# Performance work log

Hardware: AMD Instinct MI355X
Metric: run time of the kernel (lower is better)

Reference implementation:

```python
import jax, jax.numpy as jnp
import numpy as np

HIDDEN = 4096
N_HEADS = 32
N_KV_HEADS = 8
HEAD_DIM = 128
ROPE_THETA = 10000.0


def setup_inputs() -> dict:
    key = jax.random.key(0)
    ks = jax.random.split(key, 5)
    B, S = 1, 2048
    scale = 0.02
    return {
        "hidden_states": jax.random.normal(ks[0], (B, S, HIDDEN), dtype=jnp.float32),
        "q_w": jax.random.normal(ks[1], (N_HEADS * HEAD_DIM, HIDDEN), dtype=jnp.float32) * scale,
        "k_w": jax.random.normal(ks[2], (N_KV_HEADS * HEAD_DIM, HIDDEN), dtype=jnp.float32) * scale,
        "v_w": jax.random.normal(ks[3], (N_KV_HEADS * HEAD_DIM, HIDDEN), dtype=jnp.float32) * scale,
        "o_w": jax.random.normal(ks[4], (HIDDEN, N_HEADS * HEAD_DIM), dtype=jnp.float32) * scale,
        "position_ids": jnp.arange(S, dtype=jnp.int64 if jax.config.jax_enable_x64 else jnp.int32)[None, :],
    }


def _rotate_half(x):
    h = x.shape[-1] // 2
    return jnp.concatenate((-x[..., h:], x[..., :h]), axis=-1)


def _rope_cos_sin(position_ids, dtype):
    # default rope: inv_freq = theta^(-arange(0,hd,2)/hd), attention_scaling = 1
    inv_freq = 1.0 / (ROPE_THETA ** (jnp.arange(0, HEAD_DIM, 2, dtype=jnp.float32) / HEAD_DIM))
    freqs = position_ids.astype(jnp.float32)[:, :, None] * inv_freq[None, None, :]  # [B,S,hd/2]
    emb = jnp.concatenate((freqs, freqs), axis=-1)  # [B,S,hd]
    return jnp.cos(emb).astype(dtype), jnp.sin(emb).astype(dtype)


def reference(hidden_states, q_w, k_w, v_w, o_w, position_ids):
    B, S, _ = hidden_states.shape
    n_rep = N_HEADS // N_KV_HEADS

    q = (hidden_states @ q_w.T).reshape(B, S, N_HEADS, HEAD_DIM).transpose(0, 2, 1, 3)
    k = (hidden_states @ k_w.T).reshape(B, S, N_KV_HEADS, HEAD_DIM).transpose(0, 2, 1, 3)
    v = (hidden_states @ v_w.T).reshape(B, S, N_KV_HEADS, HEAD_DIM).transpose(0, 2, 1, 3)

    cos, sin = _rope_cos_sin(position_ids, hidden_states.dtype)
    cos = cos[:, None, :, :]  # unsqueeze head dim
    sin = sin[:, None, :, :]
    q = q * cos + _rotate_half(q) * sin
    k = k * cos + _rotate_half(k) * sin

    # repeat_kv (GQA)
    k = jnp.repeat(k, n_rep, axis=1)  # [B,H,S,hd]
    v = jnp.repeat(v, n_rep, axis=1)

    scale = HEAD_DIM ** -0.5
    scores = jnp.einsum("bhqd,bhkd->bhqk", q, k) * scale  # [B,H,S,S]
    causal = jnp.tril(jnp.ones((S, S), dtype=bool))
    scores = jnp.where(causal[None, None, :, :], scores, jnp.finfo(scores.dtype).min)
    probs = jax.nn.softmax(scores, axis=-1)
    attn = jnp.einsum("bhqk,bhkd->bhqd", probs, v)  # [B,H,S,hd]

    attn = attn.transpose(0, 2, 1, 3).reshape(B, S, N_HEADS * HEAD_DIM)
    return attn @ o_w.T
```

## Files before the change

### kernel.cpp

```cpp
#include <hip/hip_runtime.h>
#include <hip/hip_bf16.h>

#define NH   32
#define NKV  8
#define HD   128
#define SL   2048
#define HID  4096
#define KVW  1024
#define QKVN 6144

typedef __attribute__((ext_vector_type(8))) short short8;
typedef __attribute__((ext_vector_type(4))) float f32x4;

static __device__ __forceinline__ unsigned short f2bf(float f){
  union { float f; unsigned int i; } v; v.f = f;
  unsigned int r = v.i + 0x7FFFu + ((v.i >> 16) & 1u);
  return (unsigned short)(r >> 16);
}
static __device__ __forceinline__ float bf2f(unsigned short u){
  union { unsigned int i; float f; } v; v.i = ((unsigned int)u) << 16; return v.f;
}
static __device__ __forceinline__ unsigned int pack2(float lo, float hi){
  return (unsigned int)f2bf(lo) | ((unsigned int)f2bf(hi) << 16);
}
static __device__ __forceinline__ unsigned int cvtpk(float lo, float hi){
  unsigned int d;
  asm("v_cvt_pk_bf16_f32 %0, %1, %2" : "=v"(d) : "v"(lo), "v"(hi));
  return d;
}

static __device__ __forceinline__ void gload_lds16(const void* g, void* l){
  __builtin_amdgcn_global_load_lds(
      (const __attribute__((address_space(1))) void*)g,
      (__attribute__((address_space(3))) void*)l,
      16, 0, 0);
}

struct CastSegs {
  const float* src[5];
  unsigned short* dst[5];
  int off[6];
};
__global__ void cast_all(CastSegs cs, int total8){
  int stride = gridDim.x * blockDim.x;
  for (int i = blockIdx.x * blockDim.x + threadIdx.x; i < total8; i += stride){
    int s = 0;
#pragma unroll
    for (int t = 1; t < 5; ++t) s += (i >= cs.off[t]) ? 1 : 0;
    int j = i - cs.off[s];
    const float4* sp = (const float4*)cs.src[s];
    float4 a = sp[2*j + 0];
    float4 b = sp[2*j + 1];
    uint4 o;
    o.x = pack2(a.x, a.y); o.y = pack2(a.z, a.w);
    o.z = pack2(b.x, b.y); o.w = pack2(b.z, b.w);
    ((uint4*)cs.dst[s])[j] = o;
  }
}

__global__ void rope_table_kernel(const int* __restrict__ pos, float2* __restrict__ tab){
  int i = blockIdx.x * blockDim.x + threadIdx.x;
  if (i >= SL * 64) return;
  int s = i >> 6, f = i & 63;
  float inv = expf(-((float)(2 * f) / 128.0f) * 9.210340371976184f);
  float ang = (float)pos[s] * inv;
  float sn, cs;
  sincosf(ang, &sn, &cs);
  tab[i] = make_float2(cs, sn);
}

__global__ void rope_apply_kernel(unsigned short* x, const float2* __restrict__ tab,
                                  int nheads, int rowstride){
  int i = blockIdx.x * blockDim.x + threadIdx.x;
  int total = SL * nheads * 8;
  if (i >= total) return;
  int fb = (i & 7) * 8;
  int t = i >> 3;
  int h = t % nheads;
  int s = t / nheads;
  size_t base = (size_t)s * rowstride + h * HD;
  short8 x1 = *(const short8*)&x[base + fb];
  short8 x2 = *(const short8*)&x[base + fb + 64];
  const float2* tb = &tab[s * 64 + fb];
  short8 o1, o2;
#pragma unroll
  for (int j = 0; j < 8; ++j){
    float2 cs = tb[j];
    float a = bf2f((unsigned short)x1[j]);
    float b = bf2f((unsigned short)x2[j]);
    o1[j] = (short)f2bf(a * cs.x - b * cs.y);
    o2[j] = (short)f2bf(b * cs.x + a * cs.y);
  }
  *(short8*)&x[base + fb]      = o1;
  *(short8*)&x[base + fb + 64] = o2;
}

template<int BN, bool F32OUT>
__global__ __launch_bounds__(256) void gemm_bt(
  const unsigned short* __restrict__ A,
  const unsigned short* __restrict__ B,
  void* __restrict__ Cp, int M, int N, int K)
{
  constexpr int NFR = BN / 32;
  __shared__ __align__(16) unsigned short As[2][128 * 32];
  __shared__ __align__(16) unsigned short Bs[2][BN * 32];
  const int tid = threadIdx.x;
  const int lane = tid & 63, wid = tid >> 6;
  const int g = lane >> 4, c15 = lane & 15;
  const int wr = wid >> 1, wc = wid & 1;

  const int gx = gridDim.x, gy = gridDim.y;
  const int nwg = gx * gy;
  const int lin = blockIdx.y * gx + blockIdx.x;
  int mb, nb;
  const int cpx = nwg >> 3;
  const int RN  = cpx >> 3;
  if (RN > 0 && (gy & 7) == 0 && (cpx & 7) == 0 && gx % RN == 0 && (8 % (gx / RN)) == 0){
    int xcd = lin & 7, j = lin >> 3;
    int nrc = gx / RN;
    int rr = xcd / nrc, rc = xcd % nrc;
    mb = rr * 8 + (j & 7);
    nb = rc * RN + (j >> 3);
  } else { mb = lin / gx; nb = lin % gx; }
  const int m0 = mb * 128, n0 = nb * BN;

  const int srowA = wid * 32 + (lane >> 2);
  const int srowB = wid * (BN / 4) + (lane >> 2);
  const int scol  = (lane & 3) * 8;
  const unsigned short* Ag = &A[(size_t)(m0 + srowA) * K + scol];
  const unsigned short* Bg = &B[(size_t)(n0 + srowB) * K + scol];
  const size_t K16 = (size_t)16 * K;

  f32x4 acc[4][NFR] = {};

  gload_lds16(Ag,       &As[0][wid * 1024]);
  gload_lds16(Ag + K16, &As[0][wid * 1024 + 512]);
#pragma unroll
  for (int q = 0; q < BN / 64; ++q)
    gload_lds16(Bg + q * K16, &Bs[0][wid * (BN / 4) * 32 + q * 512]);
  __syncthreads();

  const int nk = K >> 5;
  for (int t = 0; t < nk; ++t){
    const int cur = t & 1;
    if (t + 1 < nk){
      const unsigned short* a2 = Ag + (size_t)(t + 1) * 32;
      const unsigned short* b2 = Bg + (size_t)(t + 1) * 32;
      const int nb2 = cur ^ 1;
      gload_lds16(a2,       &As[nb2][wid * 1024]);
      gload_lds16(a2 + K16, &As[nb2][wid * 1024 + 512]);
#pragma unroll
      for (int q = 0; q < BN / 64; ++q)
        gload_lds16(b2 + q * K16, &Bs[nb2][wid * (BN / 4) * 32 + q * 512]);
    }
    short8 af[4], bfr[NFR];
#pragma unroll
    for (int m = 0; m < 4; ++m)
      af[m] = *(const short8*)(&As[cur][(wr * 64 + m * 16 + c15) * 32 + g * 8]);
#pragma unroll
    for (int n = 0; n < NFR; ++n)
      bfr[n] = *(const short8*)(&Bs[cur][(wc * (BN / 2) + n * 16 + c15) * 32 + g * 8]);
#pragma unroll
    for (int m = 0; m < 4; ++m)
#pragma unroll
      for (int n = 0; n < NFR; ++n)
        acc[m][n] = __builtin_amdgcn_mfma_f32_16x16x32_bf16(af[m], bfr[n], acc[m][n], 0, 0, 0);
    __syncthreads();
  }

#pragma unroll
  for (int m = 0; m < 4; ++m)
#pragma unroll
    for (int n = 0; n < NFR; ++n){
      int row = m0 + wr * 64 + m * 16 + g * 4;
      int col = n0 + wc * (BN / 2) + n * 16 + c15;
      f32x4 v = acc[m][n];
      if (F32OUT){
        float* C = (float*)Cp;
#pragma unroll
        for (int r = 0; r < 4; ++r) C[(size_t)(row + r) * N + col] = v[r];
      } else {
        unsigned short* C = (unsigned short*)Cp;
#pragma unroll
        for (int r = 0; r < 4; ++r) C[(size_t)(row + r) * N + col] = f2bf(v[r]);
      }
    }
}

__global__ void transpose_v_kernel(const unsigned short* __restrict__ v, int vstride,
                                   unsigned short* __restrict__ vt){
  __shared__ unsigned short t[64][65];
  int h  = blockIdx.z;
  int d0 = blockIdx.y * 64;
  int s0 = blockIdx.x * 64;
  int c  = threadIdx.x & 63;
  int r0 = threadIdx.x >> 6;
#pragma unroll
  for (int r = r0; r < 64; r += 4) t[r][c] = v[(size_t)(s0 + r) * vstride + h * HD + d0 + c];
  __syncthreads();
#pragma unroll
  for (int r = r0; r < 64; r += 4) vt[(size_t)(h * HD + d0 + r) * SL + s0 + c] = t[c][r];
}

__global__ __launch_bounds__(512, 4) void flash_attn_kernel(
  const unsigned short* __restrict__ Q,
  const unsigned short* __restrict__ Kb,
  const unsigned short* __restrict__ Vt,
  unsigned short* __restrict__ O)
{
  __shared__ __align__(16) unsigned short Ks[2][64 * 128];
  __shared__ __align__(16) unsigned short Vs[2][128 * 64];
  const int tid = threadIdx.x, lane = tid & 63, wid = tid >> 6;
  const int g = lane >> 4, c15 = lane & 15;
  const int kvh = blockIdx.x;
  const int yy = blockIdx.y;
  const int qb = (yy < 32) ? (63 - yy) : (yy - 32);
  const int h = kvh * 4 + (wid & 3);
  const int rg = wid >> 2;
  const int q0 = qb * 32;
  const int qg = q0 + rg * 16 + c15;
  const int qmax = q0 + rg * 16 + 15;

  short8 aq[4];
  {
    size_t qrow = (size_t)qg * QKVN + h * HD;
#pragma unroll
    for (int kk = 0; kk < 4; ++kk)
      aq[kk] = *(const short8*)(&Q[qrow + kk * 32 + g * 8]);
  }

  const int krow = tid >> 3, kcol = (tid & 7) * 8;
  const int vrow = tid >> 2, vcol = (tid & 3) * 8;
  const unsigned short* Kgb = Kb + (size_t)kvh * HD;
  const unsigned short* Vgb = Vt + ((size_t)kvh * HD + vrow) * SL;

  auto loadKV = [&](int kt, uint4& a, uint4& b, uint4& c, uint4& d){
    const unsigned short* kg = Kgb + (size_t)(kt * 64 + krow) * QKVN + kcol;
    a = *(const uint4*)kg; b = *(const uint4*)(kg + 64);
    const unsigned short* vg = Vgb + kt * 64 + vcol;
    c = *(const uint4*)vg; d = *(const uint4*)(vg + 32);
  };
  auto writeKV = [&](int buf, uint4 a, uint4 b, uint4 c, uint4 d){
    *(uint4*)((char*)&Ks[buf][0] + krow * 256 + (( kcol * 2       ) ^ ((krow & 7) << 4))) = a;
    *(uint4*)((char*)&Ks[buf][0] + krow * 256 + (((kcol * 2) + 128) ^ ((krow & 7) << 4))) = b;
    *(uint4*)((char*)&Vs[buf][0] + vrow * 128 + (( vcol * 2       ) ^ ((vrow & 7) << 4))) = c;
    *(uint4*)((char*)&Vs[buf][0] + vrow * 128 + (((vcol * 2) +  64) ^ ((vrow & 7) << 4))) = d;
  };

  float m_i = -1e30f, l_i = 0.f;
  f32x4 oacc[8];
#pragma unroll
  for (int df = 0; df < 8; ++df) oacc[df] = (f32x4){0.f, 0.f, 0.f, 0.f};

  const float scl2 = 0.08838834764831845f * 1.4426950408889634f;
  const int nt = (q0 + 31) / 64 + 1;

  uint4 kr0, kr1, vr0, vr1;
  loadKV(0, kr0, kr1, vr0, vr1);
  writeKV(0, kr0, kr1, vr0, vr1);
  if (nt > 1) loadKV(1, kr0, kr1, vr0, vr1);
  __syncthreads();

  for (int kt = 0; kt < nt; ++kt){
    const int cur = kt & 1, nxt = cur ^ 1;
    if (kt + 1 < nt) writeKV(nxt, kr0, kr1, vr0, vr1);
    if (kt + 2 < nt) loadKV(kt + 2, kr0, kr1, vr0, vr1);

    f32x4 sc[4];
    __builtin_amdgcn_s_setprio(1);
#pragma unroll
    for (int f = 0; f < 4; ++f){
      sc[f] = (f32x4){0.f, 0.f, 0.f, 0.f};
      if (kt * 64 + f * 16 <= qmax){
#pragma unroll
        for (int kk = 0; kk < 4; ++kk){
          short8 bk = *(const short8*)((const char*)&Ks[cur][0] + (f * 16 + c15) * 256 +
                                       ((kk * 64 + g * 16) ^ ((c15 & 7) << 4)));
          sc[f] = __builtin_amdgcn_mfma_f32_16x16x32_bf16(bk, aq[kk], sc[f], 0, 0, 0);
        }
      }
    }
    __builtin_amdgcn_s_setprio(0);

    float p[4][4];
    if (kt * 64 + 63 <= q0 + rg * 16){
#pragma unroll
      for (int f = 0; f < 4; ++f)
#pragma unroll
        for (int r = 0; r < 4; ++r) p[f][r] = sc[f][r] * scl2;
    } else {
#pragma unroll
      for (int f = 0; f < 4; ++f)
#pragma unroll
        for (int r = 0; r < 4; ++r){
          int kvg = kt * 64 + f * 16 + g * 4 + r;
          p[f][r] = (kvg <= qg) ? sc[f][r] * scl2 : -1e30f;
        }
    }

    float mf[4];
#pragma unroll
    for (int f = 0; f < 4; ++f)
      mf[f] = fmaxf(fmaxf(p[f][0], p[f][1]), fmaxf(p[f][2], p[f][3]));
    float pmax = fmaxf(fmaxf(mf[0], mf[1]), fmaxf(mf[2], mf[3]));
    pmax = fmaxf(pmax, __shfl_xor(pmax, 16, 64));
    pmax = fmaxf(pmax, __shfl_xor(pmax, 32, 64));

    if (!__all(pmax - m_i <= 8.0f)){
      float mnew = fmaxf(m_i, pmax);
      float cf = exp2f(m_i - mnew);
      float cfr[4];
#pragma unroll
      for (int r = 0; r < 4; ++r) cfr[r] = __shfl(cf, (lane & 48) | (g * 4 + r), 64);
#pragma unroll
      for (int df = 0; df < 8; ++df)
#pragma unroll
        for (int r = 0; r < 4; ++r) oacc[df][r] *= cfr[r];
      l_i *= cf;
      m_i = mnew;
    }

    float sf[4];
#pragma unroll
    for (int f = 0; f < 4; ++f){
#pragma unroll
      for (int r = 0; r < 4; ++r) p[f][r] = exp2f(p[f][r] - m_i);
      sf[f] = (p[f][0] + p[f][1]) + (p[f][2] + p[f][3]);
    }
    float lsum = (sf[0] + sf[1]) + (sf[2] + sf[3]);
    lsum += __shfl_xor(lsum, 16, 64);
    lsum += __shfl_xor(lsum, 32, 64);
    l_i += lsum;

    unsigned int pd[4][2];
#pragma unroll
    for (int f = 0; f < 4; ++f){
      pd[f][0] = cvtpk(p[f][0], p[f][1]);
      pd[f][1] = cvtpk(p[f][2], p[f][3]);
    }

    const int src0 = ((g & 1) << 5) | c15;
    const int src1 = src0 + 16;
    const bool hiF = (g >= 2);
#pragma unroll
    for (int kk = 0; kk < 2; ++kk){
      if (kt * 64 + kk * 32 <= qmax){
        union { unsigned int u[4]; short8 s8; } pa;
#pragma unroll
        for (int pr = 0; pr < 2; ++pr){
          unsigned int a0 = __shfl((int)pd[2 * kk + 0][pr], src0, 64);
          unsigned int b0 = __shfl((int)pd[2 * kk + 1][pr], src0, 64);
          unsigned int a1 = __shfl((int)pd[2 * kk + 0][pr], src1, 64);
          unsigned int b1 = __shfl((int)pd[2 * kk + 1][pr], src1, 64);
          pa.u[pr]     = hiF ? b0 : a0;
          pa.u[2 + pr] = hiF ? b1 : a1;
        }
        __builtin_amdgcn_s_setprio(1);
#pragma unroll
        for (int df = 0; df < 8; ++df){
          short8 bv = *(const short8*)((const char*)&Vs[cur][0] + (df * 16 + c15) * 128 +
                                       ((kk * 64 + g * 16) ^ ((c15 & 7) << 4)));
          oacc[df] = __builtin_amdgcn_mfma_f32_16x16x32_bf16(pa.s8, bv, oacc[df], 0, 0, 0);
        }
        __builtin_amdgcn_s_setprio(0);
      }
    }
    __syncthreads();
  }

  float lr[4];
#pragma unroll
  for (int r = 0; r < 4; ++r) lr[r] = __shfl(l_i, (lane & 48) | (g * 4 + r), 64);
#pragma unroll
  for (int df = 0; df < 8; ++df)
#pragma unroll
    for (int r = 0; r < 4; ++r){
      int row = q0 + rg * 16 + g * 4 + r;
      O[(size_t)row * HID + h * HD + df * 16 + c15] = f2bf(oacc[df][r] / lr[r]);
    }
}

extern "C" void kernel_launch(void* const* d_in, const int* in_sizes, int n_in,
                              void* d_out, int out_size, void* d_ws, size_t ws_size,
                              hipStream_t stream)
{
  const float* hs  = (const float*)d_in[0];
  const float* qw  = (const float*)d_in[1];
  const float* kw  = (const float*)d_in[2];
  const float* vw  = (const float*)d_in[3];
  const float* ow  = (const float*)d_in[4];
  const int*   pos = (const int*)d_in[5];

  char* w = (char*)d_ws;
  auto alloc = [&](size_t bytes){ char* p = w; w += (bytes + 255) & ~(size_t)255; return p; };
  unsigned short* xb   = (unsigned short*)alloc((size_t)SL * HID * 2);
  unsigned short* wqkv = (unsigned short*)alloc((size_t)QKVN * HID * 2);
  unsigned short* owb  = (unsigned short*)alloc((size_t)HID * HID * 2);
  unsigned short* qkv  = (unsigned short*)alloc((size_t)SL * QKVN * 2);
  unsigned short* vt   = (unsigned short*)alloc((size_t)SL * KVW * 2);
  unsigned short* ab   = (unsigned short*)alloc((size_t)SL * HID * 2);
  float2*         tab  = (float2*)alloc((size_t)SL * 64 * sizeof(float2));

  CastSegs cs;
  cs.src[0] = hs;  cs.dst[0] = xb;
  cs.src[1] = qw;  cs.dst[1] = wqkv;
  cs.src[2] = kw;  cs.dst[2] = wqkv + (size_t)HID * HID;
  cs.src[3] = vw;  cs.dst[3] = wqkv + (size_t)(HID + KVW) * HID;
  cs.src[4] = ow;  cs.dst[4] = owb;
  int n8s[5] = { SL * HID / 8, HID * HID / 8, KVW * HID / 8, KVW * HID / 8, HID * HID / 8 };
  cs.off[0] = 0;
  for (int i = 0; i < 5; ++i) cs.off[i + 1] = cs.off[i] + n8s[i];
  int total8 = cs.off[5];
  cast_all<<<2048, 256, 0, stream>>>(cs, total8);

  rope_table_kernel<<<(SL * 64 + 255) / 256, 256, 0, stream>>>(pos, tab);

  gemm_bt<128, false><<<dim3(QKVN / 128, SL / 128), 256, 0, stream>>>(xb, wqkv, qkv, SL, QKVN, HID);

  rope_apply_kernel<<<(SL * 40 * 8 + 255) / 256, 256, 0, stream>>>(qkv, tab, 40, QKVN);

  transpose_v_kernel<<<dim3(SL / 64, HD / 64, NKV), 256, 0, stream>>>(qkv + HID + KVW, QKVN, vt);

  flash_attn_kernel<<<dim3(NKV, SL / 32), 512, 0, stream>>>(qkv, qkv + HID, vt, ab);

  gemm_bt<128, true><<<dim3(HID / 128, SL / 128), 256, 0, stream>>>(ab, owb, d_out, SL, HID, HID);
}
```

Baseline: 339.0 us.

## Triple-buffer GEMM LDS stages with explicit vmcnt waits and MFMA priority

Moves the bf16 GEMM main loop from double to triple LDS buffering, so global-to-LDS loads are issued two K-steps ahead. The full __syncthreads is replaced by raw s_barrier calls plus hand-written s_waitcnt vmcnt counts, which wait only for the tile about to be consumed. The MFMA block runs under s_setprio(1) to favour math issue. The goal is to hide global load latency better and cut barrier stalls, at the cost of more LDS per block, which may lower occupancy. The vmcnt constants assume a fixed number of loads per stage, and that may not match every BN instantiation.

```diff
diff --git a/kernel.cpp b/kernel.cpp
--- a/kernel.cpp
+++ b/kernel.cpp
@@ -102,8 +102,8 @@
   void* __restrict__ Cp, int M, int N, int K)
 {
   constexpr int NFR = BN / 32;
-  __shared__ __align__(16) unsigned short As[2][128 * 32];
-  __shared__ __align__(16) unsigned short Bs[2][BN * 32];
+  __shared__ __align__(16) unsigned short As[3][128 * 32];
+  __shared__ __align__(16) unsigned short Bs[3][BN * 32];
   const int tid = threadIdx.x;
   const int lane = tid & 63, wid = tid >> 6;
   const int g = lane >> 4, c15 = lane & 15;
@@ -131,28 +131,36 @@
   const unsigned short* Bg = &B[(size_t)(n0 + srowB) * K + scol];
   const size_t K16 = (size_t)16 * K;
 
+  auto stage = [&](int t){
+    const int b = t % 3;
+    const unsigned short* a2 = Ag + (size_t)t * 32;
+    const unsigned short* b2 = Bg + (size_t)t * 32;
+    gload_lds16(a2,       &As[b][wid * 1024]);
+    gload_lds16(a2 + K16, &As[b][wid * 1024 + 512]);
+#pragma unroll
+    for (int q = 0; q < BN / 64; ++q)
+      gload_lds16(b2 + q * K16, &Bs[b][wid * (BN / 4) * 32 + q * 512]);
+  };
+
   f32x4 acc[4][NFR] = {};
 
-  gload_lds16(Ag,       &As[0][wid * 1024]);
-  gload_lds16(Ag + K16, &As[0][wid * 1024 + 512]);
-#pragma unroll
-  for (int q = 0; q < BN / 64; ++q)
-    gload_lds16(Bg + q * K16, &Bs[0][wid * (BN / 4) * 32 + q * 512]);
-  __syncthreads();
+  stage(0);
+  stage(1);
 
   const int nk = K >> 5;
   for (int t = 0; t < nk; ++t){
-    const int cur = t & 1;
-    if (t + 1 < nk){
-      const unsigned short* a2 = Ag + (size_t)(t + 1) * 32;
-      const unsigned short* b2 = Bg + (size_t)(t + 1) * 32;
-      const int nb2 = cur ^ 1;
-      gload_lds16(a2,       &As[nb2][wid * 1024]);
-      gload_lds16(a2 + K16, &As[nb2][wid * 1024 + 512]);
-#pragma unroll
-      for (int q = 0; q < BN / 64; ++q)
-        gload_lds16(b2 + q * K16, &Bs[nb2][wid * (BN / 4) * 32 + q * 512]);
-    }
+    const int cur = t % 3;
+    __builtin_amdgcn_s_barrier();
+    if (t + 2 < nk){
+      stage(t + 2);
+      asm volatile("s_waitcnt vmcnt(8)" ::: "memory");
+    } else if (t + 1 < nk){
+      asm volatile("s_waitcnt vmcnt(4)" ::: "memory");
+    } else {
+      asm volatile("s_waitcnt vmcnt(0)" ::: "memory");
+    }
+    __builtin_amdgcn_s_barrier();
+
     short8 af[4], bfr[NFR];
 #pragma unroll
     for (int m = 0; m < 4; ++m)
@@ -160,12 +168,13 @@
 #pragma unroll
     for (int n = 0; n < NFR; ++n)
       bfr[n] = *(const short8*)(&Bs[cur][(wc * (BN / 2) + n * 16 + c15) * 32 + g * 8]);
+    __builtin_amdgcn_s_setprio(1);
 #pragma unroll
     for (int m = 0; m < 4; ++m)
 #pragma unroll
       for (int n = 0; n < NFR; ++n)
         acc[m][n] = __builtin_amdgcn_mfma_f32_16x16x32_bf16(af[m], bfr[n], acc[m][n], 0, 0, 0);
-    __syncthreads();
+    __builtin_amdgcn_s_setprio(0);
   }
 
 #pragma unroll
```

Result: no change. 344.9 us (+1.7%).
